# Optimization experiments

Hardware: AMD Instinct MI355X
Metric: run time of the kernel (lower is better)

The kernel has to match this reference:

```python
import jax, jax.numpy as jnp
import numpy as np

H, NH, QLORA, KVLORA, DN, DR, DV = 2048, 16, 1536, 512, 128, 64, 128
QD = DN + DR  # 192
EPS = 1e-6
ROPE_BASE = 10000.0


def rmsnorm(x, g):
    var = jnp.mean(x * x, axis=-1, keepdims=True)
    return x * jax.lax.rsqrt(var + EPS) * g


def rotate_half(x):
    x1, x2 = jnp.split(x, 2, axis=-1)
    return jnp.concatenate([-x2, x1], axis=-1)


def rope_cos_sin(seq_len):
    inv_freq = 1.0 / (ROPE_BASE ** (jnp.arange(0, DR, 2, dtype=jnp.float32) / DR))
    t = jnp.arange(seq_len, dtype=jnp.float32)
    freqs = jnp.outer(t, inv_freq)           # [S, DR/2]
    emb = jnp.concatenate([freqs, freqs], -1)  # [S, DR]
    return jnp.cos(emb), jnp.sin(emb)


def setup_inputs() -> dict:
    key = jax.random.key(0)
    ks = jax.random.split(key, 6)
    B, S = 2, 2048
    sc = 0.02
    return {
        "hidden_states": jax.random.normal(ks[0], (B, S, H), jnp.float32),
        "w_qa": jax.random.normal(ks[1], (QLORA, H), jnp.float32) * sc,
        "g_qa": jnp.ones((QLORA,), jnp.float32),
        "w_qb": jax.random.normal(ks[2], (NH * QD, QLORA), jnp.float32) * sc,
        "w_kva": jax.random.normal(ks[3], (KVLORA + DR, H), jnp.float32) * sc,
        "g_kva": jnp.ones((KVLORA,), jnp.float32),
        "w_kvb": jax.random.normal(ks[4], (NH * (DN + DV), KVLORA), jnp.float32) * sc,
        "w_o": jax.random.normal(ks[5], (H, NH * DV), jnp.float32) * sc,
    }


def reference(hidden_states, w_qa, g_qa, w_qb, w_kva, g_kva, w_kvb, w_o):
    B, S, _ = hidden_states.shape
    # Q path: low-rank down-proj -> RMSNorm -> up-proj
    q_a = hidden_states @ w_qa.T                        # [B,S,QLORA]
    q = rmsnorm(q_a, g_qa) @ w_qb.T                     # [B,S,NH*QD]
    q = q.reshape(B, S, NH, QD).transpose(0, 2, 1, 3)   # [B,NH,S,QD]
    q_nope, q_pe = q[..., :DN], q[..., DN:]
    # KV path: joint down-proj with MQA rope slice
    ckv = hidden_states @ w_kva.T                       # [B,S,KVLORA+DR]
    compressed_kv, k_pe = ckv[..., :KVLORA], ckv[..., KVLORA:]
    k_pe = k_pe.reshape(B, S, 1, DR).transpose(0, 2, 1, 3)  # [B,1,S,DR]
    kv = rmsnorm(compressed_kv, g_kva) @ w_kvb.T        # [B,S,NH*(DN+DV)]
    kv = kv.reshape(B, S, NH, DN + DV).transpose(0, 2, 1, 3)
    k_nope, v = kv[..., :DN], kv[..., DN:]              # [B,NH,S,DN], [B,NH,S,DV]
    # decoupled RoPE on rope sub-dims only
    cos, sin = rope_cos_sin(S)                          # [S,DR]
    cos = cos[None, None]; sin = sin[None, None]
    q_pe = q_pe * cos + rotate_half(q_pe) * sin
    k_pe = k_pe * cos + rotate_half(k_pe) * sin
    query = jnp.concatenate([q_nope, q_pe], -1)         # [B,NH,S,QD]
    key = jnp.concatenate([k_nope, jnp.broadcast_to(k_pe, (B, NH, S, DR))], -1)
    # causal SDPA with scale = QD**-0.5
    scale = QD ** (-0.5)
    scores = jnp.einsum("bhsd,bhtd->bhst", query, key) * scale
    mask = jnp.tril(jnp.ones((S, S), bool))
    scores = jnp.where(mask, scores, jnp.finfo(scores.dtype).min)
    attn = jax.nn.softmax(scores, axis=-1)
    out = jnp.einsum("bhst,bhtd->bhsd", attn, v)        # [B,NH,S,DV]
    out = out.transpose(0, 2, 1, 3).reshape(B, S, NH * DV)
    return out @ w_o.T
```

## Files before the change

### kernel.cpp

```cpp
#include <hip/hip_runtime.h>
#include <cstdint>
#include <cstring>

typedef short short8 __attribute__((ext_vector_type(8)));
typedef float float4v __attribute__((ext_vector_type(4)));
typedef float float4g __attribute__((ext_vector_type(4)));
typedef unsigned short ushort4v __attribute__((ext_vector_type(4)));
typedef unsigned int uint2v __attribute__((ext_vector_type(2)));

typedef __attribute__((address_space(3))) unsigned int lds_uint;
typedef __attribute__((address_space(1))) const unsigned int glob_uint;

static __device__ __forceinline__ void async16(void* lds, const void* g) {
    __builtin_amdgcn_global_load_lds((glob_uint*)g, (lds_uint*)lds, 16, 0, 0);
}

static __device__ __forceinline__ float b2f(unsigned short u) {
    unsigned int x = ((unsigned int)u) << 16;
    float f;
    __builtin_memcpy(&f, &x, 4);
    return f;
}
static __device__ __forceinline__ unsigned short f2b(float f) {
    unsigned int x;
    __builtin_memcpy(&x, &f, 4);
    unsigned int r = (x + 0x7fffu + ((x >> 16) & 1u)) >> 16;
    return (unsigned short)r;
}

__global__ __launch_bounds__(256) void k_f2b6(
    const float* __restrict__ s0, unsigned short* __restrict__ d0,
    const float* __restrict__ s1, unsigned short* __restrict__ d1,
    const float* __restrict__ s2, unsigned short* __restrict__ d2,
    const float* __restrict__ s3, unsigned short* __restrict__ d3,
    const float* __restrict__ s4, unsigned short* __restrict__ d4,
    const float* __restrict__ s5, unsigned short* __restrict__ d5,
    float qs) {
    int blk = blockIdx.x;
    const float* s; unsigned short* d; float sc = 1.f; int rel;
    if (blk < 8192)       { s = s0; d = d0; rel = blk; }
    else if (blk < 11264) { s = s1; d = d1; rel = blk - 8192; }
    else if (blk < 15872) { s = s2; d = d2; rel = blk - 11264; sc = qs; }
    else if (blk < 17024) { s = s3; d = d3; rel = blk - 15872; }
    else if (blk < 19072) { s = s4; d = d4; rel = blk - 17024; }
    else                  { s = s5; d = d5; rel = blk - 19072; }
    int i = (rel * 256 + threadIdx.x) * 4;
    float4g v = *(const float4g*)(s + i);
    ushort4v r;
    r.x = f2b(v.x * sc); r.y = f2b(v.y * sc); r.z = f2b(v.z * sc); r.w = f2b(v.w * sc);
    *(ushort4v*)(d + i) = r;
}

static __device__ __forceinline__ void gemm_bt_body(
    const unsigned short* __restrict__ A, int lda,
    const unsigned short* __restrict__ W,
    void* __restrict__ C, int ldc,
    int N, int K, int c_fp32, int bx, int by) {
    __shared__ __align__(16) unsigned short As[128 * 32];
    __shared__ __align__(16) unsigned short Ws[128 * 32];
    const int tid = threadIdx.x;
    const int m0 = by * 128, n0 = bx * 128;
    const int wave = tid >> 6, lane = tid & 63;
    const int wm = (wave >> 1) * 64, wn = (wave & 1) * 64;
    const int lrow = lane & 15, quad = lane >> 4;
    const int srow = lane >> 2, spiece = lane & 3;

    float4v acc[4][4];
    float4v z = {0.f, 0.f, 0.f, 0.f};
#pragma unroll
    for (int i = 0; i < 4; i++)
#pragma unroll
        for (int j = 0; j < 4; j++) acc[i][j] = z;

    for (int k0 = 0; k0 < K; k0 += 32) {
#pragma unroll
        for (int ii = 0; ii < 2; ++ii) {
            int i = wave + ii * 4;
            int row = i * 16 + srow;
            async16(&As[i * 512], &A[(size_t)(m0 + row) * lda + k0 + spiece * 8]);
            int wr = n0 + row;
            if (wr > N - 1) wr = N - 1;
            async16(&Ws[i * 512], &W[(size_t)wr * K + k0 + spiece * 8]);
        }
        __syncthreads();
        short8 af[4], bfr[4];
#pragma unroll
        for (int i = 0; i < 4; i++)
            af[i] = *(const short8*)&As[(wm + i * 16 + lrow) * 32 + quad * 8];
#pragma unroll
        for (int i = 0; i < 4; i++)
            bfr[i] = *(const short8*)&Ws[(wn + i * 16 + lrow) * 32 + quad * 8];
#pragma unroll
        for (int i = 0; i < 4; i++)
#pragma unroll
            for (int j = 0; j < 4; j++)
                acc[i][j] = __builtin_amdgcn_mfma_f32_16x16x32_bf16(af[i], bfr[j], acc[i][j], 0, 0, 0);
        __syncthreads();
    }

    const int rbase = quad * 4;
#pragma unroll
    for (int i = 0; i < 4; i++) {
#pragma unroll
        for (int j = 0; j < 4; j++) {
            int col = n0 + wn + j * 16 + lrow;
            if (col >= N) continue;
#pragma unroll
            for (int r = 0; r < 4; r++) {
                int row = m0 + wm + i * 16 + rbase + r;
                float v = acc[i][j][r];
                if (c_fp32)
                    ((float*)C)[(size_t)row * ldc + col] = v;
                else
                    ((unsigned short*)C)[(size_t)row * ldc + col] = f2b(v);
            }
        }
    }
}

__global__ __launch_bounds__(256, 3)
void k_gemm_bt(const unsigned short* __restrict__ A, int lda,
               const unsigned short* __restrict__ W,
               void* __restrict__ C, int ldc,
               int N, int K, int c_fp32) {
    gemm_bt_body(A, lda, W, C, ldc, N, K, c_fp32, blockIdx.x, blockIdx.y);
}

__global__ __launch_bounds__(256, 3)
void k_gemm_dual(const unsigned short* __restrict__ A0, int lda0,
                 const unsigned short* __restrict__ W0, void* __restrict__ C0,
                 int ldc0, int N0, int K0, int nbx0,
                 const unsigned short* __restrict__ A1, int lda1,
                 const unsigned short* __restrict__ W1, void* __restrict__ C1,
                 int ldc1, int N1, int K1) {
    int bx = blockIdx.x;
    if (bx < nbx0) {
        gemm_bt_body(A0, lda0, W0, C0, ldc0, N0, K0, 0, bx, blockIdx.y);
    } else {
        gemm_bt_body(A1, lda1, W1, C1, ldc1, N1, K1, 0, bx - nbx0, blockIdx.y);
    }
}

__global__ __launch_bounds__(192) void k_norm2(
    unsigned short* __restrict__ qa, const float* __restrict__ g_qa,
    unsigned short* __restrict__ ckv, const float* __restrict__ g_kva) {
    __shared__ float wsum[3];
    int blk = blockIdx.x;
    int tid = threadIdx.x;
    if (blk < 4096) {
        size_t base = (size_t)blk * 1536 + tid * 8;
        short8 v8 = *(const short8*)(qa + base);
        float vf[8];
        float ss = 0.f;
#pragma unroll
        for (int i = 0; i < 8; i++) {
            vf[i] = b2f((unsigned short)v8[i]);
            ss += vf[i] * vf[i];
        }
        for (int off = 32; off > 0; off >>= 1) ss += __shfl_xor(ss, off);
        int wave = tid >> 6, lane = tid & 63;
        if (lane == 0) wsum[wave] = ss;
        __syncthreads();
        ss = wsum[0] + wsum[1] + wsum[2];
        float scale = rsqrtf(ss * (1.f / 1536.f) + 1e-6f);
        short8 r8;
#pragma unroll
        for (int i = 0; i < 8; i++) r8[i] = (short)f2b(vf[i] * scale * g_qa[tid * 8 + i]);
        *(short8*)(qa + base) = r8;
    } else {
        int row = blk - 4096;
        if (tid < 64) {
            size_t base = (size_t)row * 576 + tid * 8;
            short8 v8 = *(const short8*)(ckv + base);
            float vf[8];
            float ss = 0.f;
#pragma unroll
            for (int i = 0; i < 8; i++) {
                vf[i] = b2f((unsigned short)v8[i]);
                ss += vf[i] * vf[i];
            }
            for (int off = 32; off > 0; off >>= 1) ss += __shfl_xor(ss, off);
            float scale = rsqrtf(ss * (1.f / 512.f) + 1e-6f);
            short8 r8;
#pragma unroll
            for (int i = 0; i < 8; i++) r8[i] = (short)f2b(vf[i] * scale * g_kva[tid * 8 + i]);
            *(short8*)(ckv + base) = r8;
        } else if (tid < 96) {
            int d = tid - 64;
            int s = row & 2047;
            size_t base = (size_t)row * 576 + 512;
            float inv = exp2f((float)d * -0.4152410118609203f);
            float f = (float)s * inv;
            float c, sn;
            sincosf(f, &sn, &c);
            float x1 = b2f(ckv[base + d]), x2 = b2f(ckv[base + d + 32]);
            ckv[base + d] = f2b(x1 * c - x2 * sn);
            ckv[base + d + 32] = f2b(x2 * c + x1 * sn);
        }
    }
}

__global__ __launch_bounds__(256) void k_transpose_v(const unsigned short* __restrict__ kv,
                                                     unsigned short* __restrict__ vt) {
    int bh = blockIdx.z;
    int b = bh >> 4, h = bh & 15;
    int s0 = blockIdx.x * 32, d0 = blockIdx.y * 32;
    __shared__ unsigned short t[32][33];
    int tx = threadIdx.x & 31, ty = threadIdx.x >> 5;
#pragma unroll
    for (int i = 0; i < 4; i++) {
        int s = s0 + ty + i * 8;
        t[ty + i * 8][tx] = kv[(size_t)(b * 2048 + s) * 4096 + h * 256 + 128 + d0 + tx];
    }
    __syncthreads();
#pragma unroll
    for (int i = 0; i < 4; i++) {
        int d = d0 + ty + i * 8;
        vt[((size_t)bh * 128 + d) * 2048 + s0 + tx] = t[tx][ty + i * 8];
    }
}

__global__ __launch_bounds__(256, 1)
void k_attn8(const unsigned short* __restrict__ q,
             const unsigned short* __restrict__ kv,
             const unsigned short* __restrict__ ckv,
             const unsigned short* __restrict__ vt,
             unsigned short* __restrict__ ao)
{
    __shared__ __align__(16) unsigned short Ks[2][12288];
    __shared__ __align__(16) unsigned short Vs[2][8192];
    __shared__ __align__(16) unsigned short Pl[4][1280];

    const int pb = blockIdx.x >> 5;
    const int bh = blockIdx.x & 31;
    const int b = bh >> 4, h = bh & 15;
    const int tid = threadIdx.x, wave = tid >> 6, lane = tid & 63;
    const int lrow = lane & 15, quad = lane >> 4;
    const int srow = lane >> 2, spiece = lane & 3;
    unsigned short* Pw = Pl[wave];

    const int colx = spiece ^ ((srow >> 1) & 3);
    const int qx = (quad ^ ((lrow >> 1) & 3)) * 8;

    float invf[8];
#pragma unroll
    for (int j = 0; j < 8; j++)
        invf[j] = exp2f((float)(quad * 8 + j) * -0.4152410118609203f);

    short8 ones;
#pragma unroll
    for (int j = 0; j < 8; j++) ones[j] = (short)0x3F80;

    float4v z4 = {0.f, 0.f, 0.f, 0.f};

    auto stageK = [&](int kt, int buf) {
        const int kb = kt * 64;
#pragma unroll
        for (int ii = 0; ii < 6; ++ii) {
            int id = wave * 6 + ii;
            int ks = id >> 2;
            int row = (id & 3) * 16 + srow;
            int key = b * 2048 + kb + row;
            const unsigned short* g =
                (ks < 4) ? kv + (size_t)key * 4096 + h * 256 + ks * 32 + colx * 8
                         : ckv + (size_t)key * 576 + 512 + (ks - 4) * 32 + colx * 8;
            async16(&Ks[buf][id * 512], g);
        }
    };
    auto stageV = [&](int kt, int buf) {
        const int kb = kt * 64;
#pragma unroll
        for (int ii = 0; ii < 4; ++ii) {
            int id = wave * 4 + ii;
            int d = (id & 7) * 16 + srow;
            const unsigned short* g =
                vt + ((size_t)bh * 128 + d) * 2048 + kb + (id >> 3) * 32 + colx * 8;
            async16(&Vs[buf][id * 512], g);
        }
    };

    for (int pass = 0; pass < 2; ++pass) {
        const int qt = pass ? (15 - pb) : pb;
        const int tok0 = b * 2048 + qt * 128;
        const int nk = 2 * qt + 2;

        short8 qf[2][6];
#pragma unroll
        for (int mi = 0; mi < 2; mi++) {
            int row = wave * 32 + mi * 16 + lrow;
            const unsigned short* qp = q + (size_t)(tok0 + row) * 3072 + h * 192;
#pragma unroll
            for (int ks = 0; ks < 6; ks++) qf[mi][ks] = *(const short8*)(qp + ks * 32 + quad * 8);
            float sp = (float)(qt * 128 + row);
#pragma unroll
            for (int j = 0; j < 8; j++) {
                float f = sp * invf[j];
                float c, sn;
                sincosf(f, &sn, &c);
                float x1 = b2f((unsigned short)qf[mi][4][j]);
                float x2 = b2f((unsigned short)qf[mi][5][j]);
                qf[mi][4][j] = (short)f2b(x1 * c - x2 * sn);
                qf[mi][5][j] = (short)f2b(x2 * c + x1 * sn);
            }
        }

        float m_st[2];
        m_st[0] = m_st[1] = -__builtin_inff();
        float4v o[2][8], osum[2];
#pragma unroll
        for (int mi = 0; mi < 2; mi++) {
            osum[mi] = z4;
#pragma unroll
            for (int dt = 0; dt < 8; dt++) o[mi][dt] = z4;
        }

        __syncthreads();
        stageK(0, 0);
        stageV(0, 0);

        for (int kt = 0; kt < nk; ++kt) {
            __syncthreads();
            if (kt + 1 < nk) {
                stageK(kt + 1, (kt + 1) & 1);
                stageV(kt + 1, (kt + 1) & 1);
            }
            const unsigned short* Kb = Ks[kt & 1];
            const unsigned short* Vb = Vs[kt & 1];
            const int kb = kt * 64;

            float4v sc[2][4];
#pragma unroll
            for (int mi = 0; mi < 2; mi++)
#pragma unroll
                for (int nt = 0; nt < 4; nt++) sc[mi][nt] = z4;
            __builtin_amdgcn_s_setprio(1);
#pragma unroll
            for (int ks = 0; ks < 6; ks++) {
#pragma unroll
                for (int nt = 0; nt < 4; nt++) {
                    short8 kf = *(const short8*)&Kb[ks * 2048 + nt * 512 + lrow * 32 + qx];
                    sc[0][nt] = __builtin_amdgcn_mfma_f32_16x16x32_bf16(kf, qf[0][ks], sc[0][nt], 0, 0, 0);
                    sc[1][nt] = __builtin_amdgcn_mfma_f32_16x16x32_bf16(kf, qf[1][ks], sc[1][nt], 0, 0, 0);
                }
            }
            __builtin_amdgcn_s_setprio(0);

            if (kt >= nk - 2) {
#pragma unroll
                for (int mi = 0; mi < 2; mi++) {
                    int rowc = qt * 128 + wave * 32 + mi * 16 + lrow;
#pragma unroll
                    for (int nt = 0; nt < 4; nt++)
#pragma unroll
                        for (int r = 0; r < 4; r++) {
                            int keyc = kb + nt * 16 + quad * 4 + r;
                            if (keyc > rowc) sc[mi][nt][r] = -__builtin_inff();
                        }
                }
            }

            float mx[2];
#pragma unroll
            for (int mi = 0; mi < 2; mi++) {
                float m = sc[mi][0][0];
#pragma unroll
                for (int nt = 0; nt < 4; nt++)
#pragma unroll
                    for (int r = 0; r < 4; r++) m = fmaxf(m, sc[mi][nt][r]);
                m = fmaxf(m, __shfl_xor(m, 16));
                m = fmaxf(m, __shfl_xor(m, 32));
                mx[mi] = m;
            }
            bool within = (mx[0] <= m_st[0] + 6.f) && (mx[1] <= m_st[1] + 6.f);
            if (!__all(within)) {
                float alpha[2];
#pragma unroll
                for (int mi = 0; mi < 2; mi++) {
                    float mnew = fmaxf(m_st[mi], mx[mi]);
                    alpha[mi] = exp2f(m_st[mi] - mnew);
                    m_st[mi] = mnew;
                }
                float arow[2][4];
#pragma unroll
                for (int mi = 0; mi < 2; mi++)
#pragma unroll
                    for (int r = 0; r < 4; r++) arow[mi][r] = __shfl(alpha[mi], quad * 4 + r);
#pragma unroll
                for (int mi = 0; mi < 2; mi++) {
#pragma unroll
                    for (int r = 0; r < 4; r++) osum[mi][r] *= arow[mi][r];
#pragma unroll
                    for (int dt = 0; dt < 8; dt++)
#pragma unroll
                        for (int r = 0; r < 4; r++) o[mi][dt][r] *= arow[mi][r];
                }
            }
            uint2v pk[2][4];
#pragma unroll
            for (int mi = 0; mi < 2; mi++) {
#pragma unroll
                for (int nt = 0; nt < 4; nt++) {
                    float p0 = exp2f(sc[mi][nt][0] - m_st[mi]);
                    float p1 = exp2f(sc[mi][nt][1] - m_st[mi]);
                    float p2 = exp2f(sc[mi][nt][2] - m_st[mi]);
                    float p3 = exp2f(sc[mi][nt][3] - m_st[mi]);
                    pk[mi][nt].x = (unsigned int)f2b(p0) | ((unsigned int)f2b(p1) << 16);
                    pk[mi][nt].y = (unsigned int)f2b(p2) | ((unsigned int)f2b(p3) << 16);
                }
            }

#pragma unroll
            for (int ks2 = 0; ks2 < 2; ks2++) {
#pragma unroll
                for (int mi = 0; mi < 2; mi++) {
                    int row = mi * 16 + lrow;
                    *(uint2v*)&Pw[row * 40 + quad * 4] = pk[mi][ks2 * 2];
                    *(uint2v*)&Pw[row * 40 + 16 + quad * 4] = pk[mi][ks2 * 2 + 1];
                }
                short8 pa0 = *(const short8*)&Pw[lrow * 40 + quad * 8];
                short8 pa1 = *(const short8*)&Pw[(16 + lrow) * 40 + quad * 8];
                __builtin_amdgcn_s_setprio(1);
#pragma unroll
                for (int dt = 0; dt < 8; dt++) {
                    short8 vf = *(const short8*)&Vb[(ks2 * 8 + dt) * 512 + lrow * 32 + qx];
                    o[0][dt] = __builtin_amdgcn_mfma_f32_16x16x32_bf16(pa0, vf, o[0][dt], 0, 0, 0);
                    o[1][dt] = __builtin_amdgcn_mfma_f32_16x16x32_bf16(pa1, vf, o[1][dt], 0, 0, 0);
                }
                osum[0] = __builtin_amdgcn_mfma_f32_16x16x32_bf16(pa0, ones, osum[0], 0, 0, 0);
                osum[1] = __builtin_amdgcn_mfma_f32_16x16x32_bf16(pa1, ones, osum[1], 0, 0, 0);
                __builtin_amdgcn_s_setprio(0);
            }
        }

#pragma unroll
        for (int mi = 0; mi < 2; mi++) {
#pragma unroll
            for (int r = 0; r < 4; r++) {
                float linv = 1.f / osum[mi][r];
                unsigned short* dst =
                    ao + (size_t)(tok0 + wave * 32 + mi * 16 + quad * 4 + r) * 2048 + h * 128;
#pragma unroll
                for (int dt = 0; dt < 8; dt++) dst[dt * 16 + lrow] = f2b(o[mi][dt][r] * linv);
            }
        }
    }
}

extern "C" void kernel_launch(void* const* d_in, const int* in_sizes, int n_in,
                              void* d_out, int out_size, void* d_ws, size_t ws_size,
                              hipStream_t stream) {
    (void)in_sizes; (void)n_in; (void)out_size; (void)ws_size;
    const float* hs    = (const float*)d_in[0];
    const float* w_qa  = (const float*)d_in[1];
    const float* g_qa  = (const float*)d_in[2];
    const float* w_qb  = (const float*)d_in[3];
    const float* w_kva = (const float*)d_in[4];
    const float* g_kva = (const float*)d_in[5];
    const float* w_kvb = (const float*)d_in[6];
    const float* w_o   = (const float*)d_in[7];

    char* ws = (char*)d_ws;
    size_t off = 0;
    auto alloc = [&](size_t bytes) -> unsigned short* {
        unsigned short* p = (unsigned short*)(ws + off);
        off += (bytes + 255) & ~(size_t)255;
        return p;
    };
    unsigned short* hb    = alloc(4096ull * 2048 * 2);
    unsigned short* wqa   = alloc(1536ull * 2048 * 2);
    unsigned short* wqb   = alloc(3072ull * 1536 * 2);
    unsigned short* wkva  = alloc(576ull * 2048 * 2);
    unsigned short* wkvb  = alloc(4096ull * 512 * 2);
    unsigned short* wo    = alloc(2048ull * 2048 * 2);
    unsigned short* qa    = alloc(4096ull * 1536 * 2);
    unsigned short* ckv   = alloc(4096ull * 576 * 2);
    unsigned short* qbuf  = alloc(4096ull * 3072 * 2);
    unsigned short* kvbuf = alloc(4096ull * 4096 * 2);
    unsigned short* vtb   = alloc(32ull * 128 * 2048 * 2);
    unsigned short* ao    = alloc(4096ull * 2048 * 2);

    const float qscale = 0.07216878364870323f * 1.4426950408889634f;

    k_f2b6<<<dim3(23168), dim3(256), 0, stream>>>(
        hs, hb, w_qa, wqa, w_qb, wqb, w_kva, wkva, w_kvb, wkvb, w_o, wo, qscale);

    k_gemm_dual<<<dim3(17, 32), 256, 0, stream>>>(
        hb, 2048, wqa, qa, 1536, 1536, 2048, 12,
        hb, 2048, wkva, ckv, 576, 576, 2048);

    k_norm2<<<dim3(8192), dim3(192), 0, stream>>>(qa, g_qa, ckv, g_kva);

    k_gemm_dual<<<dim3(56, 32), 256, 0, stream>>>(
        qa, 1536, wqb, qbuf, 3072, 3072, 1536, 24,
        ckv, 576, wkvb, kvbuf, 4096, 4096, 512);

    k_transpose_v<<<dim3(64, 4, 32), 256, 0, stream>>>(kvbuf, vtb);
    k_attn8<<<dim3(256), 256, 0, stream>>>(qbuf, kvbuf, ckv, vtb, ao);
    k_gemm_bt<<<dim3(16, 32), 256, 0, stream>>>(ao, 2048, wo, d_out, 2048, 2048, 2048, 1);
}
```

Measured before the change: 452.8 us.

## Split attention work into one q-tile per block with two blocks per CU

```diff
diff --git a/kernel.cpp b/kernel.cpp
--- a/kernel.cpp
+++ b/kernel.cpp
@@ -220,38 +220,67 @@
     }
 }
 
-__global__ __launch_bounds__(256, 1)
-void k_attn8(const unsigned short* __restrict__ q,
+__global__ __launch_bounds__(256, 2)
+void k_attn9(const unsigned short* __restrict__ q,
              const unsigned short* __restrict__ kv,
              const unsigned short* __restrict__ ckv,
              const unsigned short* __restrict__ vt,
              unsigned short* __restrict__ ao)
 {
     __shared__ __align__(16) unsigned short Ks[2][12288];
-    __shared__ __align__(16) unsigned short Vs[2][8192];
+    __shared__ __align__(16) unsigned short Vs[8192];
     __shared__ __align__(16) unsigned short Pl[4][1280];
 
-    const int pb = blockIdx.x >> 5;
-    const int bh = blockIdx.x & 31;
+    const int lb = blockIdx.x;
+    const int qt = (lb < 256) ? (lb >> 5) : 15 - ((lb & 255) >> 5);
+    const int bh = lb & 31;
     const int b = bh >> 4, h = bh & 15;
     const int tid = threadIdx.x, wave = tid >> 6, lane = tid & 63;
     const int lrow = lane & 15, quad = lane >> 4;
     const int srow = lane >> 2, spiece = lane & 3;
+    const int tok0 = b * 2048 + qt * 128;
     unsigned short* Pw = Pl[wave];
 
     const int colx = spiece ^ ((srow >> 1) & 3);
     const int qx = (quad ^ ((lrow >> 1) & 3)) * 8;
 
-    float invf[8];
-#pragma unroll
-    for (int j = 0; j < 8; j++)
-        invf[j] = exp2f((float)(quad * 8 + j) * -0.4152410118609203f);
+    short8 qf[2][6];
+#pragma unroll
+    for (int mi = 0; mi < 2; mi++) {
+        int row = wave * 32 + mi * 16 + lrow;
+        const unsigned short* qp = q + (size_t)(tok0 + row) * 3072 + h * 192;
+#pragma unroll
+        for (int ks = 0; ks < 6; ks++) qf[mi][ks] = *(const short8*)(qp + ks * 32 + quad * 8);
+        float sp = (float)(qt * 128 + row);
+#pragma unroll
+        for (int j = 0; j < 8; j++) {
+            float inv = exp2f((float)(quad * 8 + j) * -0.4152410118609203f);
+            float f = sp * inv;
+            float c, sn;
+            sincosf(f, &sn, &c);
+            float x1 = b2f((unsigned short)qf[mi][4][j]);
+            float x2 = b2f((unsigned short)qf[mi][5][j]);
+            qf[mi][4][j] = (short)f2b(x1 * c - x2 * sn);
+            qf[mi][5][j] = (short)f2b(x2 * c + x1 * sn);
+        }
+    }
 
     short8 ones;
 #pragma unroll
     for (int j = 0; j < 8; j++) ones[j] = (short)0x3F80;
 
+    float m_st[2];
+    m_st[0] = m_st[1] = -__builtin_inff();
     float4v z4 = {0.f, 0.f, 0.f, 0.f};
+    float4v o[2][8], osum[2];
+#pragma unroll
+    for (int mi = 0; mi < 2; mi++) {
+        osum[mi] = z4;
+#pragma unroll
+        for (int dt = 0; dt < 8; dt++) o[mi][dt] = z4;
+    }
+
+    const int nk = 2 * qt + 2;
 
     auto stageK = [&](int kt, int buf) {
         const int kb = kt * 64;
@@ -267,7 +296,7 @@
             async16(&Ks[buf][id * 512], g);
         }
     };
-    auto stageV = [&](int kt, int buf) {
+    auto stageV = [&](int kt) {
         const int kb = kt * 64;
 #pragma unroll
         for (int ii = 0; ii < 4; ++ii) {
@@ -275,173 +304,134 @@
             int d = (id & 7) * 16 + srow;
             const unsigned short* g =
                 vt + ((size_t)bh * 128 + d) * 2048 + kb + (id >> 3) * 32 + colx * 8;
-            async16(&Vs[buf][id * 512], g);
+            async16(&Vs[id * 512], g);
         }
     };
 
-    for (int pass = 0; pass < 2; ++pass) {
-        const int qt = pass ? (15 - pb) : pb;
-        const int tok0 = b * 2048 + qt * 128;
-        const int nk = 2 * qt + 2;
-
-        short8 qf[2][6];
+    stageK(0, 0);
+
+    for (int kt = 0; kt < nk; ++kt) {
+        __syncthreads();
+        stageV(kt);
+        if (kt + 1 < nk) stageK(kt + 1, (kt + 1) & 1);
+        const unsigned short* Kb = Ks[kt & 1];
+        const int kb = kt * 64;
+
+        float4v sc[2][4];
+#pragma unroll
+        for (int mi = 0; mi < 2; mi++)
+#pragma unroll
+            for (int nt = 0; nt < 4; nt++) sc[mi][nt] = z4;
+        __builtin_amdgcn_s_setprio(1);
+#pragma unroll
+        for (int ks = 0; ks < 6; ks++) {
+#pragma unroll
+            for (int nt = 0; nt < 4; nt++) {
+                short8 kf = *(const short8*)&Kb[ks * 2048 + nt * 512 + lrow * 32 + qx];
+                sc[0][nt] = __builtin_amdgcn_mfma_f32_16x16x32_bf16(kf, qf[0][ks], sc[0][nt], 0, 0, 0);
+                sc[1][nt] = __builtin_amdgcn_mfma_f32_16x16x32_bf16(kf, qf[1][ks], sc[1][nt], 0, 0, 0);
+            }
+        }
+        __builtin_amdgcn_s_setprio(0);
+
+        if (kt >= nk - 2) {
+#pragma unroll
+            for (int mi = 0; mi < 2; mi++) {
+                int rowc = qt * 128 + wave * 32 + mi * 16 + lrow;
+#pragma unroll
+                for (int nt = 0; nt < 4; nt++)
+#pragma unroll
+                    for (int r = 0; r < 4; r++) {
+                        int keyc = kb + nt * 16 + quad * 4 + r;
+                        if (keyc > rowc) sc[mi][nt][r] = -__builtin_inff();
+                    }
+            }
+        }
+
+        float mx[2];
 #pragma unroll
         for (int mi = 0; mi < 2; mi++) {
-            int row = wave * 32 + mi * 16 + lrow;
-            const unsigned short* qp = q + (size_t)(tok0 + row) * 3072 + h * 192;
-#pragma unroll
-            for (int ks = 0; ks < 6; ks++) qf[mi][ks] = *(const short8*)(qp + ks * 32 + quad * 8);
-            float sp = (float)(qt * 128 + row);
-#pragma unroll
-            for (int j = 0; j < 8; j++) {
-                float f = sp * invf[j];
-                float c, sn;
-                sincosf(f, &sn, &c);
-                float x1 = b2f((unsigned short)qf[mi][4][j]);
-                float x2 = b2f((unsigned short)qf[mi][5][j]);
-                qf[mi][4][j] = (short)f2b(x1 * c - x2 * sn);
-                qf[mi][5][j] = (short)f2b(x2 * c + x1 * sn);
-            }
-        }
-
-        float m_st[2];
-        m_st[0] = m_st[1] = -__builtin_inff();
-        float4v o[2][8], osum[2];
+            float m = sc[mi][0][0];
+#pragma unroll
+            for (int nt = 0; nt < 4; nt++)
+#pragma unroll
+                for (int r = 0; r < 4; r++) m = fmaxf(m, sc[mi][nt][r]);
+            m = fmaxf(m, __shfl_xor(m, 16));
+            m = fmaxf(m, __shfl_xor(m, 32));
+            mx[mi] = m;
+        }
+        bool within = (mx[0] <= m_st[0] + 6.f) && (mx[1] <= m_st[1] + 6.f);
+        if (!__all(within)) {
+            float alpha[2];
+#pragma unroll
+            for (int mi = 0; mi < 2; mi++) {
+                float mnew = fmaxf(m_st[mi], mx[mi]);
+                alpha[mi] = exp2f(m_st[mi] - mnew);
+                m_st[mi] = mnew;
+            }
+            float arow[2][4];
+#pragma unroll
+            for (int mi = 0; mi < 2; mi++)
+#pragma unroll
+                for (int r = 0; r < 4; r++) arow[mi][r] = __shfl(alpha[mi], quad * 4 + r);
+#pragma unroll
+            for (int mi = 0; mi < 2; mi++) {
+#pragma unroll
+                for (int r = 0; r < 4; r++) osum[mi][r] *= arow[mi][r];
+#pragma unroll
+                for (int dt = 0; dt < 8; dt++)
+#pragma unroll
+                    for (int r = 0; r < 4; r++) o[mi][dt][r] *= arow[mi][r];
+            }
+        }
+        uint2v pk[2][4];
 #pragma unroll
         for (int mi = 0; mi < 2; mi++) {
-            osum[mi] = z4;
-#pragma unroll
-            for (int dt = 0; dt < 8; dt++) o[mi][dt] = z4;
+#pragma unroll
+            for (int nt = 0; nt < 4; nt++) {
+                float p0 = exp2f(sc[mi][nt][0] - m_st[mi]);
+                float p1 = exp2f(sc[mi][nt][1] - m_st[mi]);
+                float p2 = exp2f(sc[mi][nt][2] - m_st[mi]);
+                float p3 = exp2f(sc[mi][nt][3] - m_st[mi]);
+                pk[mi][nt].x = (unsigned int)f2b(p0) | ((unsigned int)f2b(p1) << 16);
+                pk[mi][nt].y = (unsigned int)f2b(p2) | ((unsigned int)f2b(p3) << 16);
+            }
         }
 
         __syncthreads();
-        stageK(0, 0);
-        stageV(0, 0);
-
-        for (int kt = 0; kt < nk; ++kt) {
-            __syncthreads();
-            if (kt + 1 < nk) {
-                stageK(kt + 1, (kt + 1) & 1);
-                stageV(kt + 1, (kt + 1) & 1);
-            }
-            const unsigned short* Kb = Ks[kt & 1];
-            const unsigned short* Vb = Vs[kt & 1];
-            const int kb = kt * 64;
-
-            float4v sc[2][4];
-#pragma unroll
-            for (int mi = 0; mi < 2; mi++)
-#pragma unroll
-                for (int nt = 0; nt < 4; nt++) sc[mi][nt] = z4;
+
+#pragma unroll
+        for (int ks2 = 0; ks2 < 2; ks2++) {
+#pragma unroll
+            for (int mi = 0; mi < 2; mi++) {
+                int row = mi * 16 + lrow;
+                *(uint2v*)&Pw[row * 40 + quad * 4] = pk[mi][ks2 * 2];
+                *(uint2v*)&Pw[row * 40 + 16 + quad * 4] = pk[mi][ks2 * 2 + 1];
+            }
+            short8 pa0 = *(const short8*)&Pw[lrow * 40 + quad * 8];
+            short8 pa1 = *(const short8*)&Pw[(16 + lrow) * 40 + quad * 8];
             __builtin_amdgcn_s_setprio(1);
 #pragma unroll
-            for (int ks = 0; ks < 6; ks++) {
-#pragma unroll
-                for (int nt = 0; nt < 4; nt++) {
-                    short8 kf = *(const short8*)&Kb[ks * 2048 + nt * 512 + lrow * 32 + qx];
-                    sc[0][nt] = __builtin_amdgcn_mfma_f32_16x16x32_bf16(kf, qf[0][ks], sc[0][nt], 0, 0, 0);
-                    sc[1][nt] = __builtin_amdgcn_mfma_f32_16x16x32_bf16(kf, qf[1][ks], sc[1][nt], 0, 0, 0);
-                }
-            }
+            for (int dt = 0; dt < 8; dt++) {
+                short8 vf = *(const short8*)&Vs[(ks2 * 8 + dt) * 512 + lrow * 32 + qx];
+                o[0][dt] = __builtin_amdgcn_mfma_f32_16x16x32_bf16(pa0, vf, o[0][dt], 0, 0, 0);
+                o[1][dt] = __builtin_amdgcn_mfma_f32_16x16x32_bf16(pa1, vf, o[1][dt], 0, 0, 0);
+            }
+            osum[0] = __builtin_amdgcn_mfma_f32_16x16x32_bf16(pa0, ones, osum[0], 0, 0, 0);
+            osum[1] = __builtin_amdgcn_mfma_f32_16x16x32_bf16(pa1, ones, osum[1], 0, 0, 0);
             __builtin_amdgcn_s_setprio(0);
-
-            if (kt >= nk - 2) {
-#pragma unroll
-                for (int mi = 0; mi < 2; mi++) {
-                    int rowc = qt * 128 + wave * 32 + mi * 16 + lrow;
-#pragma unroll
-                    for (int nt = 0; nt < 4; nt++)
-#pragma unroll
-                        for (int r = 0; r < 4; r++) {
-                            int keyc = kb + nt * 16 + quad * 4 + r;
-                            if (keyc > rowc) sc[mi][nt][r] = -__builtin_inff();
-                        }
-                }
-            }
-
-            float mx[2];
-#pragma unroll
-            for (int mi = 0; mi < 2; mi++) {
-                float m = sc[mi][0][0];
-#pragma unroll
-                for (int nt = 0; nt < 4; nt++)
-#pragma unroll
-                    for (int r = 0; r < 4; r++) m = fmaxf(m, sc[mi][nt][r]);
-                m = fmaxf(m, __shfl_xor(m, 16));
-                m = fmaxf(m, __shfl_xor(m, 32));
-                mx[mi] = m;
-            }
-            bool within = (mx[0] <= m_st[0] + 6.f) && (mx[1] <= m_st[1] + 6.f);
-            if (!__all(within)) {
-                float alpha[2];
-#pragma unroll
-                for (int mi = 0; mi < 2; mi++) {
-                    float mnew = fmaxf(m_st[mi], mx[mi]);
-                    alpha[mi] = exp2f(m_st[mi] - mnew);
-                    m_st[mi] = mnew;
-                }
-                float arow[2][4];
-#pragma unroll
-                for (int mi = 0; mi < 2; mi++)
-#pragma unroll
-                    for (int r = 0; r < 4; r++) arow[mi][r] = __shfl(alpha[mi], quad * 4 + r);
-#pragma unroll
-                for (int mi = 0; mi < 2; mi++) {
-#pragma unroll
-                    for (int r = 0; r < 4; r++) osum[mi][r] *= arow[mi][r];
-#pragma unroll
-                    for (int dt = 0; dt < 8; dt++)
-#pragma unroll
-                        for (int r = 0; r < 4; r++) o[mi][dt][r] *= arow[mi][r];
-                }
-            }
-            uint2v pk[2][4];
-#pragma unroll
-            for (int mi = 0; mi < 2; mi++) {
-#pragma unroll
-                for (int nt = 0; nt < 4; nt++) {
-                    float p0 = exp2f(sc[mi][nt][0] - m_st[mi]);
-                    float p1 = exp2f(sc[mi][nt][1] - m_st[mi]);
-                    float p2 = exp2f(sc[mi][nt][2] - m_st[mi]);
-                    float p3 = exp2f(sc[mi][nt][3] - m_st[mi]);
-                    pk[mi][nt].x = (unsigned int)f2b(p0) | ((unsigned int)f2b(p1) << 16);
-                    pk[mi][nt].y = (unsigned int)f2b(p2) | ((unsigned int)f2b(p3) << 16);
-                }
-            }
-
-#pragma unroll
-            for (int ks2 = 0; ks2 < 2; ks2++) {
-#pragma unroll
-                for (int mi = 0; mi < 2; mi++) {
-                    int row = mi * 16 + lrow;
-                    *(uint2v*)&Pw[row * 40 + quad * 4] = pk[mi][ks2 * 2];
-                    *(uint2v*)&Pw[row * 40 + 16 + quad * 4] = pk[mi][ks2 * 2 + 1];
-                }
-                short8 pa0 = *(const short8*)&Pw[lrow * 40 + quad * 8];
-                short8 pa1 = *(const short8*)&Pw[(16 + lrow) * 40 + quad * 8];
-                __builtin_amdgcn_s_setprio(1);
-#pragma unroll
-                for (int dt = 0; dt < 8; dt++) {
-                    short8 vf = *(const short8*)&Vb[(ks2 * 8 + dt) * 512 + lrow * 32 + qx];
-                    o[0][dt] = __builtin_amdgcn_mfma_f32_16x16x32_bf16(pa0, vf, o[0][dt], 0, 0, 0);
-                    o[1][dt] = __builtin_amdgcn_mfma_f32_16x16x32_bf16(pa1, vf, o[1][dt], 0, 0, 0);
-                }
-                osum[0] = __builtin_amdgcn_mfma_f32_16x16x32_bf16(pa0, ones, osum[0], 0, 0, 0);
-                osum[1] = __builtin_amdgcn_mfma_f32_16x16x32_bf16(pa1, ones, osum[1], 0, 0, 0);
-                __builtin_amdgcn_s_setprio(0);
-            }
-        }
-
-#pragma unroll
-        for (int mi = 0; mi < 2; mi++) {
-#pragma unroll
-            for (int r = 0; r < 4; r++) {
-                float linv = 1.f / osum[mi][r];
-                unsigned short* dst =
-                    ao + (size_t)(tok0 + wave * 32 + mi * 16 + quad * 4 + r) * 2048 + h * 128;
-#pragma unroll
-                for (int dt = 0; dt < 8; dt++) dst[dt * 16 + lrow] = f2b(o[mi][dt][r] * linv);
-            }
+        }
+    }
+
+#pragma unroll
+    for (int mi = 0; mi < 2; mi++) {
+#pragma unroll
+        for (int r = 0; r < 4; r++) {
+            float linv = 1.f / osum[mi][r];
+            unsigned short* dst =
+                ao + (size_t)(tok0 + wave * 32 + mi * 16 + quad * 4 + r) * 2048 + h * 128;
+#pragma unroll
+            for (int dt = 0; dt < 8; dt++) dst[dt * 16 + lrow] = f2b(o[mi][dt][r] * linv);
         }
     }
 }
@@ -495,6 +485,6 @@
         ckv, 576, wkvb, kvbuf, 4096, 4096, 512);
 
     k_transpose_v<<<dim3(64, 4, 32), 256, 0, stream>>>(kvbuf, vtb);
-    k_attn8<<<dim3(256), 256, 0, stream>>>(qbuf, kvbuf, ckv, vtb, ao);
+    k_attn9<<<dim3(512), 256, 0, stream>>>(qbuf, kvbuf, ckv, vtb, ao);
     k_gemm_bt<<<dim3(16, 32), 256, 0, stream>>>(ao, 2048, wo, d_out, 2048, 2048, 2048, 1);
 }
```

After: 431.9 us. 4.6% less time.
